# Kernel optimization log

Hardware: AMD Instinct MI355X
Metric: run time of the kernel (lower is better)

The kernel has to match this reference:

```python
import jax, jax.numpy as jnp
import numpy as np

B, T, C, H = 4, 2048, 1024, 16
HD = C // H

def setup_inputs() -> dict:
    key = jax.random.key(0)
    ks = jax.random.split(key, 9)
    s = 1.0 / np.sqrt(C)
    return {
        'x':  jax.random.normal(ks[0], (B, T, C), jnp.float32),
        'Wq': jax.random.normal(ks[1], (C, C), jnp.float32) * s,
        'bq': jnp.zeros((C,), jnp.float32),
        'Wk': jax.random.normal(ks[2], (C, C), jnp.float32) * s,
        'bk': jnp.zeros((C,), jnp.float32),
        'Wv': jax.random.normal(ks[3], (C, C), jnp.float32) * s,
        'bv': jnp.zeros((C,), jnp.float32),
        'Wo': jax.random.normal(ks[4], (C, C), jnp.float32) * s,
        'bo': jnp.zeros((C,), jnp.float32),
    }

def reference(x, Wq, bq, Wk, bk, Wv, bv, Wo, bo):
    Bx, Tx, Cx = x.shape
    # projections (torch Linear: x @ W.T + b); split heads -> (B,H,T,HD)
    def heads(y):
        return y.reshape(Bx, Tx, H, HD).transpose(0, 2, 1, 3)
    q = heads(x @ Wq.T + bq)
    k = heads(x @ Wk.T + bk)
    v = heads(x @ Wv.T + bv)
    # NOTE: original scales by 1/sqrt(embedding_dim), not head_dim
    scale = 1.0 / jnp.sqrt(jnp.asarray(Cx, x.dtype))
    att = jnp.einsum('bhqd,bhkd->bhqk', q, k) * scale
    mask = jnp.tril(jnp.ones((Tx, Tx), dtype=bool))
    att = jnp.where(mask, att, jnp.asarray(-jnp.inf, att.dtype))
    att = jax.nn.softmax(att, axis=-1)
    y = jnp.einsum('bhqk,bhkd->bhqd', att, v)
    y = y.transpose(0, 2, 1, 3).reshape(Bx, Tx, Cx)
    return y @ Wo.T + bo
```

## Files before the change

kernel.cpp:

```cpp
#include <hip/hip_runtime.h>
#include <hip/hip_bf16.h>
#include <stdint.h>

#define NB 4
#define NT 2048
#define NC 1024
#define NH 16
#define NHD 64
#define NM (NB*NT)

typedef __attribute__((ext_vector_type(8))) __bf16 bf16x8;
typedef __attribute__((ext_vector_type(4))) float floatx4;
typedef __attribute__((ext_vector_type(8))) unsigned short ushortx8;

#define AS1(p) ((const __attribute__((address_space(1))) void*)(p))
#define AS3(p) ((__attribute__((address_space(3))) void*)(p))

__device__ __forceinline__ unsigned short f2bf(float f) {
    union { float f; unsigned int u; } v; v.f = f;
    unsigned int u = v.u;
    return (unsigned short)((u + 0x7FFFu + ((u >> 16) & 1u)) >> 16);
}
__device__ __forceinline__ unsigned int pk2(float lo, float hi) {
    union { float f; unsigned int u; } a, b; a.f = hi; b.f = lo;
    return __builtin_amdgcn_perm(a.u, b.u, 0x07060302u);
}


__global__ void cast_all(const float* __restrict__ x,
                         const float* __restrict__ w0, const float* __restrict__ w1,
                         const float* __restrict__ w2, const float* __restrict__ w3,
                         unsigned short* __restrict__ xo,
                         unsigned short* __restrict__ o0, unsigned short* __restrict__ o1,
                         unsigned short* __restrict__ o2, unsigned short* __restrict__ o3)
{
    const int wid  = (blockIdx.x * blockDim.x + threadIdx.x) >> 6;
    const int lane = threadIdx.x & 63;
    const float* in; unsigned short* out; int tile;
    if (wid < 16384) { in = x; out = xo; tile = wid; }
    else {
        const int t = wid - 16384;
        tile = t & 2047;
        switch (t >> 11) {
            case 0: in = w0; out = o0; break;
            case 1: in = w1; out = o1; break;
            case 2: in = w2; out = o2; break;
            default: in = w3; out = o3; break;
        }
    }
    const int R = tile >> 5, C = tile & 31;
    const float* src = in + ((size_t)(R*16 + (lane >> 2)))*1024 + C*32 + (lane & 3)*8;
    const floatx4 v0 = *(const floatx4*)src;
    const floatx4 v1 = *(const floatx4*)(src + 4);
    ushortx8 o;
    o[0] = f2bf(v0[0]); o[1] = f2bf(v0[1]); o[2] = f2bf(v0[2]); o[3] = f2bf(v0[3]);
    o[4] = f2bf(v1[0]); o[5] = f2bf(v1[1]); o[6] = f2bf(v1[2]); o[7] = f2bf(v1[3]);
    *(ushortx8*)&out[(size_t)tile*512 + (((lane & 3)*16 + (lane >> 2)))*8] = o;
}

#define TM 128
#define TN 128
#define BK 32

template<int MODE>
__device__ __forceinline__ void gemm_core(
    const unsigned short* __restrict__ A,
    const unsigned short* __restrict__ W,
    const float* __restrict__ bias,
    void* __restrict__ Out,
    unsigned short* As, unsigned short* Bs,
    int m_base, int n_base, float oscale)
{
    const int tid  = threadIdx.x;
    const int lane = tid & 63;
    const int wv   = tid >> 6;
    const int quad = lane >> 4;
    const int l16  = lane & 15;
    const int wm = (wv >> 1) * 64;
    const int wn = (wv & 1) * 64;

    floatx4 acc[4][4];
    #pragma unroll
    for (int i = 0; i < 4; ++i)
        #pragma unroll
        for (int j = 0; j < 4; ++j)
            acc[i][j] = (floatx4){0.f, 0.f, 0.f, 0.f};

    const int kct = NC >> 5;

    const unsigned short* At = A + ((size_t)((m_base >> 4) + wv*2) * kct) * 512 + (size_t)lane*8;
    const unsigned short* Wt = W + ((size_t)((n_base >> 4) + wv*2) * kct) * 512 + (size_t)lane*8;
    const size_t rstride = (size_t)kct * 512;

    #pragma unroll
    for (int i = 0; i < 2; ++i) {
        __builtin_amdgcn_global_load_lds(AS1(At + i*rstride),
                                         AS3(&As[(wv*2 + i)*512]), 16, 0, 0);
        __builtin_amdgcn_global_load_lds(AS1(Wt + i*rstride),
                                         AS3(&Bs[(wv*2 + i)*512]), 16, 0, 0);
    }

    #pragma unroll 1
    for (int kt = 0; kt < 32; ++kt) {
        const int cur = (kt & 1) << 12;
        const int nxt = 4096 - cur;
        if (kt < 31) {
            #pragma unroll
            for (int i = 0; i < 2; ++i) {
                __builtin_amdgcn_global_load_lds(
                    AS1(At + (size_t)(kt+1)*512 + i*rstride),
                    AS3(&As[nxt + (wv*2 + i)*512]), 16, 0, 0);
                __builtin_amdgcn_global_load_lds(
                    AS1(Wt + (size_t)(kt+1)*512 + i*rstride),
                    AS3(&Bs[nxt + (wv*2 + i)*512]), 16, 0, 0);
            }
            asm volatile("s_waitcnt vmcnt(4)" ::: "memory");
        } else {
            asm volatile("s_waitcnt vmcnt(0)" ::: "memory");
        }
        __builtin_amdgcn_s_barrier();

        bf16x8 af[4], bfr[4];
        #pragma unroll
        for (int mi = 0; mi < 4; ++mi)
            af[mi] = *(const bf16x8*)&As[cur + ((wv >> 1)*4 + mi)*512 + lane*8];
        #pragma unroll
        for (int ni = 0; ni < 4; ++ni)
            bfr[ni] = *(const bf16x8*)&Bs[cur + ((wv & 1)*4 + ni)*512 + lane*8];

        #pragma unroll
        for (int mi = 0; mi < 4; ++mi)
            #pragma unroll
            for (int ni = 0; ni < 4; ++ni) {
                if (MODE == 1)
                    acc[mi][ni] = __builtin_amdgcn_mfma_f32_16x16x32_bf16(
                        bfr[ni], af[mi], acc[mi][ni], 0, 0, 0);
                else
                    acc[mi][ni] = __builtin_amdgcn_mfma_f32_16x16x32_bf16(
                        af[mi], bfr[ni], acc[mi][ni], 0, 0, 0);
            }
        __builtin_amdgcn_s_barrier();
    }

    #pragma unroll
    for (int mi = 0; mi < 4; ++mi) {
        #pragma unroll
        for (int ni = 0; ni < 4; ++ni) {
            if (MODE == 0) {
                const int col = n_base + wn + ni*16 + l16;
                const float bv = bias[col & 1023];
                #pragma unroll
                for (int r = 0; r < 4; ++r) {
                    const int row = m_base + wm + mi*16 + quad*4 + r;
                    ((float*)Out)[(size_t)row * NC + col] =
                        (acc[mi][ni][r] + bv) * oscale;
                }
            } else if (MODE == 1) {
                const int d0 = n_base + wn + ni*16 + quad*4;
                const int t  = m_base + wm + mi*16 + l16;
                const float4 b4 = *(const float4*)&bias[d0];
                const int bb = t >> 11, tt = t & (NT - 1);
                const int h  = (d0 >> 6) & (NH - 1), dd0 = d0 & 63;
                const int bh = bb * NH + h;
                const size_t idx0 =
                    ((size_t)((bh*128 + (tt >> 4))*2 + (dd0 >> 5)))*512
                    + (size_t)((((dd0 >> 3) & 3)*16 + (tt & 15))*8 + (dd0 & 7));
                ushort4 st;
                st.x = f2bf((acc[mi][ni][0] + b4.x) * oscale);
                st.y = f2bf((acc[mi][ni][1] + b4.y) * oscale);
                st.z = f2bf((acc[mi][ni][2] + b4.z) * oscale);
                st.w = f2bf((acc[mi][ni][3] + b4.w) * oscale);
                *(ushort4*)&((unsigned short*)Out)[idx0] = st;
            } else {
                const int col = n_base + wn + ni*16 + l16;
                const float bv = bias[col & 1023];
                const int row0 = m_base + wm + mi*16 + quad*4;
                const int bb = row0 >> 11, t0 = row0 & (NT - 1);
                const int h  = (col >> 6) & (NH - 1), hd = col & 63;
                const int bh = bb * NH + h;
                const int tk0 = t0 & 31;
                const int qv  = (tk0 >> 2) & 3;
                const int jv0 = (tk0 >> 4) << 2;
                const size_t idx0 =
                    ((size_t)((bh*64 + (t0 >> 5))*4 + (hd >> 4)))*512
                    + (size_t)((qv*16 + (hd & 15))*8 + jv0);
                ushort4 st;
                st.x = f2bf((acc[mi][ni][0] + bv) * oscale);
                st.y = f2bf((acc[mi][ni][1] + bv) * oscale);
                st.z = f2bf((acc[mi][ni][2] + bv) * oscale);
                st.w = f2bf((acc[mi][ni][3] + bv) * oscale);
                *(ushort4*)&((unsigned short*)Out)[idx0] = st;
            }
        }
    }
}

#define QSCALE (0.03125f * 1.44269504088896340736f)

__global__ __launch_bounds__(256) void gemm_qkv(
    const unsigned short* __restrict__ A,
    const unsigned short* __restrict__ Wq, const unsigned short* __restrict__ Wk,
    const unsigned short* __restrict__ Wv,
    const float* __restrict__ bq, const float* __restrict__ bk,
    const float* __restrict__ bv,
    unsigned short* __restrict__ Qo, unsigned short* __restrict__ Ko,
    unsigned short* __restrict__ Vo)
{
    __shared__ __align__(16) unsigned short As[2*TM*BK];
    __shared__ __align__(16) unsigned short Bs[2*TN*BK];
    const int m_base = blockIdx.x * TM;
    const int n_base = blockIdx.y * TN;
    gemm_core<1>(A, Wq, bq, Qo, As, Bs, m_base, n_base, QSCALE);
    gemm_core<1>(A, Wk, bk, Ko, As, Bs, m_base, n_base, 1.0f);
    gemm_core<2>(A, Wv, bv, Vo, As, Bs, m_base, n_base, 1.0f);
}

__global__ __launch_bounds__(256) void gemm_out(
    const unsigned short* __restrict__ A,
    const unsigned short* __restrict__ W,
    const float* __restrict__ bias,
    float* __restrict__ Out)
{
    __shared__ __align__(16) unsigned short As[2*TM*BK];
    __shared__ __align__(16) unsigned short Bs[2*TN*BK];
    gemm_core<0>(A, W, bias, Out, As, Bs, blockIdx.x * TM, blockIdx.y * TN, 1.0f);
}

__device__ __forceinline__ void attn_tile(
    const bf16x8 kf[4][2], const bf16x8 vf[4][2],
    const bf16x8 q[4], floatx4 o[2][4], float l[2],
    bool diag, bool skiphi, int q0, int j0, int quad, int l16)
{
    #pragma unroll
    for (int sub = 0; sub < 2; ++sub) {
        const bf16x8 qx0 = q[sub*2];
        const bf16x8 qx1 = q[sub*2 + 1];

        floatx4 s[4];
        __builtin_amdgcn_s_setprio(1);
        #pragma unroll
        for (int ct = 0; ct < 2; ++ct) {
            s[ct] = (floatx4){0.f,0.f,0.f,0.f};
            s[ct] = __builtin_amdgcn_mfma_f32_16x16x32_bf16(kf[ct][0], qx0, s[ct], 0,0,0);
            s[ct] = __builtin_amdgcn_mfma_f32_16x16x32_bf16(kf[ct][1], qx1, s[ct], 0,0,0);
        }
        if (!skiphi) {
            #pragma unroll
            for (int ct = 2; ct < 4; ++ct) {
                s[ct] = (floatx4){0.f,0.f,0.f,0.f};
                s[ct] = __builtin_amdgcn_mfma_f32_16x16x32_bf16(kf[ct][0], qx0, s[ct], 0,0,0);
                s[ct] = __builtin_amdgcn_mfma_f32_16x16x32_bf16(kf[ct][1], qx1, s[ct], 0,0,0);
            }
        }
        __builtin_amdgcn_s_setprio(0);

        float p[4][4];
        float psum[4];
        const int row = q0 + sub*16 + l16;
        #pragma unroll
        for (int ct = 0; ct < 2; ++ct) {
            if (!diag) {
                #pragma unroll
                for (int r = 0; r < 4; ++r)
                    p[ct][r] = __builtin_amdgcn_exp2f(s[ct][r]);
            } else {
                #pragma unroll
                for (int r = 0; r < 4; ++r) {
                    const int key = j0 + ct*16 + quad*4 + r;
                    p[ct][r] = (key <= row) ? __builtin_amdgcn_exp2f(s[ct][r]) : 0.f;
                }
            }
            psum[ct] = (p[ct][0] + p[ct][1]) + (p[ct][2] + p[ct][3]);
        }
        if (!skiphi) {
            #pragma unroll
            for (int ct = 2; ct < 4; ++ct) {
                if (!diag) {
                    #pragma unroll
                    for (int r = 0; r < 4; ++r)
                        p[ct][r] = __builtin_amdgcn_exp2f(s[ct][r]);
                } else {
                    #pragma unroll
                    for (int r = 0; r < 4; ++r) {
                        const int key = j0 + ct*16 + quad*4 + r;
                        p[ct][r] = (key <= row) ? __builtin_amdgcn_exp2f(s[ct][r]) : 0.f;
                    }
                }
                psum[ct] = (p[ct][0] + p[ct][1]) + (p[ct][2] + p[ct][3]);
            }
            l[sub] += (psum[0] + psum[1]) + (psum[2] + psum[3]);
        } else {
            l[sub] += psum[0] + psum[1];
        }

        union { bf16x8 v; unsigned int u[4]; } pf0;
        pf0.u[0] = pk2(p[0][0], p[0][1]); pf0.u[1] = pk2(p[0][2], p[0][3]);
        pf0.u[2] = pk2(p[1][0], p[1][1]); pf0.u[3] = pk2(p[1][2], p[1][3]);

        __builtin_amdgcn_s_setprio(1);
        #pragma unroll
        for (int nt = 0; nt < 4; ++nt)
            o[sub][nt] = __builtin_amdgcn_mfma_f32_16x16x32_bf16(vf[nt][0], pf0.v, o[sub][nt], 0,0,0);
        __builtin_amdgcn_s_setprio(0);

        if (!skiphi) {
            union { bf16x8 v; unsigned int u[4]; } pf1;
            pf1.u[0] = pk2(p[2][0], p[2][1]); pf1.u[1] = pk2(p[2][2], p[2][3]);
            pf1.u[2] = pk2(p[3][0], p[3][1]); pf1.u[3] = pk2(p[3][2], p[3][3]);
            __builtin_amdgcn_s_setprio(1);
            #pragma unroll
            for (int nt = 0; nt < 4; ++nt)
                o[sub][nt] = __builtin_amdgcn_mfma_f32_16x16x32_bf16(vf[nt][1], pf1.v, o[sub][nt], 0,0,0);
            __builtin_amdgcn_s_setprio(0);
        }
    }
}

__device__ __forceinline__ void attn_store(
    unsigned short* __restrict__ Y, const floatx4 o[2][4], const float l[2],
    int q0, int b, int h, int quad, int l16)
{
    float la = l[0], lb = l[1];
    la += __shfl_xor(la, 16); la += __shfl_xor(la, 32);
    lb += __shfl_xor(lb, 16); lb += __shfl_xor(lb, 32);
    const float ia = 1.0f / la, ib = 1.0f / lb;
    const size_t Rbase = (size_t)((b*NT + q0) >> 4);
    const int cg = (quad >> 1), co = (quad & 1)*4;
    #pragma unroll
    for (int nt = 0; nt < 4; ++nt) {
        const size_t base = ((Rbase*32 + h*2 + (nt >> 1))*512)
                          + (size_t)((((nt & 1)*2 + cg)*16 + l16)*8 + co);
        ushort4 wa, wb;
        wa.x = f2bf(o[0][nt][0]*ia); wa.y = f2bf(o[0][nt][1]*ia);
        wa.z = f2bf(o[0][nt][2]*ia); wa.w = f2bf(o[0][nt][3]*ia);
        wb.x = f2bf(o[1][nt][0]*ib); wb.y = f2bf(o[1][nt][1]*ib);
        wb.z = f2bf(o[1][nt][2]*ib); wb.w = f2bf(o[1][nt][3]*ib);
        *(ushort4*)&Y[base]         = wa;
        *(ushort4*)&Y[base + 16384] = wb;
    }
}

__device__ __forceinline__ void attn_pair(
    const unsigned short* __restrict__ Qf,
    const unsigned short* __restrict__ Kf,
    const unsigned short* __restrict__ Vf,
    unsigned short* __restrict__ Y,
    int bh, int stA, int stB, int lane)
{
    const int quad = lane >> 4, l16 = lane & 15;
    const int b = bh >> 4, h = bh & (NH - 1);
    const int q0A = stA * 32, q0B = stB * 32;
    const int FA = q0A >> 6, FB = q0B >> 6;
    const bool skA = (q0A & 32) == 0;
    const bool skB = (q0B & 32) == 0;

    const size_t qbA = ((size_t)(bh*128 + stA*2))*1024 + (size_t)lane*8;
    const size_t qbB = ((size_t)(bh*128 + stB*2))*1024 + (size_t)lane*8;
    bf16x8 qA[4], qB[4];
    qA[0] = *(const bf16x8*)&Qf[qbA];
    qA[1] = *(const bf16x8*)&Qf[qbA + 512];
    qA[2] = *(const bf16x8*)&Qf[qbA + 1024];
    qA[3] = *(const bf16x8*)&Qf[qbA + 1536];
    qB[0] = *(const bf16x8*)&Qf[qbB];
    qB[1] = *(const bf16x8*)&Qf[qbB + 512];
    qB[2] = *(const bf16x8*)&Qf[qbB + 1024];
    qB[3] = *(const bf16x8*)&Qf[qbB + 1536];

    const unsigned short* kp = Kf + (size_t)bh*131072 + (size_t)lane*8;
    const unsigned short* vp = Vf + (size_t)bh*131072 + (size_t)lane*8;

    floatx4 oA[2][4], oB[2][4];
    float lA[2] = {0.f, 0.f}, lB[2] = {0.f, 0.f};
    #pragma unroll
    for (int s2 = 0; s2 < 2; ++s2)
        #pragma unroll
        for (int nt = 0; nt < 4; ++nt) {
            oA[s2][nt] = (floatx4){0.f,0.f,0.f,0.f};
            oB[s2][nt] = (floatx4){0.f,0.f,0.f,0.f};
        }

    for (int f = 0; f <= FB; ++f) {
        const int j0 = f * 64;
        bf16x8 kf[4][2], vf[4][2];
        const unsigned short* kt = kp + (size_t)f * 4096;
        #pragma unroll
        for (int ct = 0; ct < 4; ++ct) {
            kf[ct][0] = *(const bf16x8*)&kt[ct*1024];
            kf[ct][1] = *(const bf16x8*)&kt[ct*1024 + 512];
        }
        const unsigned short* vt = vp + (size_t)f * 4096;
        #pragma unroll
        for (int nt = 0; nt < 4; ++nt) {
            vf[nt][0] = *(const bf16x8*)&vt[nt*512];
            vf[nt][1] = *(const bf16x8*)&vt[2048 + nt*512];
        }

        if (f <= FA)
            attn_tile(kf, vf, qA, oA, lA, f == FA, (f == FA) && skA,
                      q0A, j0, quad, l16);
        attn_tile(kf, vf, qB, oB, lB, f == FB, (f == FB) && skB,
                  q0B, j0, quad, l16);
    }

    attn_store(Y, oA, lA, q0A, b, h, quad, l16);
    attn_store(Y, oB, lB, q0B, b, h, quad, l16);
}

__global__ __launch_bounds__(256, 2) void flash_attn(
    const unsigned short* __restrict__ Qf,
    const unsigned short* __restrict__ Kf,
    const unsigned short* __restrict__ Vf,
    unsigned short* __restrict__ Y)
{
    const int tid  = threadIdx.x;
    const int wave = tid >> 6;
    const int lane = tid & 63;
    const int L  = blockIdx.x;
    const int bh = (L & 7) * 8 + ((L >> 3) & 7);
    const int x  = L >> 6;
    const int w  = x * 4 + wave;
    attn_pair(Qf, Kf, Vf, Y, bh, w, 63 - w, lane);
}

extern "C" void kernel_launch(void* const* d_in, const int* in_sizes, int n_in,
                              void* d_out, int out_size, void* d_ws, size_t ws_size,
                              hipStream_t stream) {
    const float* x  = (const float*)d_in[0];
    const float* Wq = (const float*)d_in[1];
    const float* bq = (const float*)d_in[2];
    const float* Wk = (const float*)d_in[3];
    const float* bk = (const float*)d_in[4];
    const float* Wv = (const float*)d_in[5];
    const float* bv = (const float*)d_in[6];
    const float* Wo = (const float*)d_in[7];
    const float* bo = (const float*)d_in[8];

    char* ws = (char*)d_ws;
    size_t off = 0;
    auto alloc = [&](size_t bytes) -> void* {
        void* p = ws + off;
        off += (bytes + 255) & ~(size_t)255;
        return p;
    };
    unsigned short* xb  = (unsigned short*)alloc((size_t)NM * NC * 2);
    unsigned short* Wqb = (unsigned short*)alloc((size_t)NC * NC * 2);
    unsigned short* Wkb = (unsigned short*)alloc((size_t)NC * NC * 2);
    unsigned short* Wvb = (unsigned short*)alloc((size_t)NC * NC * 2);
    unsigned short* Wob = (unsigned short*)alloc((size_t)NC * NC * 2);
    unsigned short* Qb  = (unsigned short*)alloc((size_t)NM * NC * 2);
    unsigned short* Kb  = (unsigned short*)alloc((size_t)NM * NC * 2);
    unsigned short* Vtb = (unsigned short*)alloc((size_t)NM * NC * 2);
    unsigned short* Yb  = (unsigned short*)alloc((size_t)NM * NC * 2);

    cast_all<<<(24576*64)/256, 256, 0, stream>>>(
        x, Wq, Wk, Wv, Wo, xb, Wqb, Wkb, Wvb, Wob);

    gemm_qkv<<<dim3(NM / TM, NC / TN), 256, 0, stream>>>(
        xb, Wqb, Wkb, Wvb, bq, bk, bv, Qb, Kb, Vtb);

    flash_attn<<<dim3(512), 256, 0, stream>>>(Qb, Kb, Vtb, Yb);

    gemm_out<<<dim3(NM / TM, NC / TN), 256, 0, stream>>>(Yb, Wob, bo, (float*)d_out);
}
```

Before: 233.4 us.

## Triple-buffer GEMM LDS pipeline and split QKV projections across grid blocks

The GEMM core moves from double to triple buffering in LDS. Loads are issued two k-steps ahead and the vmcnt waits are adjusted so more global-to-LDS latency overlaps with the MFMA work. The QKV kernel also launches three times as many blocks, each doing one of Q, K or V instead of all three in sequence, which raises parallelism and shortens each block's tail. The larger LDS footprint (48KB per block) may lower occupancy.

```diff
diff --git a/kernel.cpp b/kernel.cpp
--- a/kernel.cpp
+++ b/kernel.cpp
@@ -93,27 +93,34 @@
     const size_t rstride = (size_t)kct * 512;
 
     #pragma unroll
-    for (int i = 0; i < 2; ++i) {
-        __builtin_amdgcn_global_load_lds(AS1(At + i*rstride),
-                                         AS3(&As[(wv*2 + i)*512]), 16, 0, 0);
-        __builtin_amdgcn_global_load_lds(AS1(Wt + i*rstride),
-                                         AS3(&Bs[(wv*2 + i)*512]), 16, 0, 0);
-    }
-
+    for (int t = 0; t < 2; ++t) {
+        #pragma unroll
+        for (int i = 0; i < 2; ++i) {
+            __builtin_amdgcn_global_load_lds(
+                AS1(At + (size_t)t*512 + i*rstride),
+                AS3(&As[t*4096 + (wv*2 + i)*512]), 16, 0, 0);
+            __builtin_amdgcn_global_load_lds(
+                AS1(Wt + (size_t)t*512 + i*rstride),
+                AS3(&Bs[t*4096 + (wv*2 + i)*512]), 16, 0, 0);
+        }
+    }
+
+    int cb = 0;
     #pragma unroll 1
     for (int kt = 0; kt < 32; ++kt) {
-        const int cur = (kt & 1) << 12;
-        const int nxt = 4096 - cur;
-        if (kt < 31) {
+        if (kt < 30) {
+            int sb = cb + 8192; if (sb >= 12288) sb -= 12288;
             #pragma unroll
             for (int i = 0; i < 2; ++i) {
                 __builtin_amdgcn_global_load_lds(
-                    AS1(At + (size_t)(kt+1)*512 + i*rstride),
-                    AS3(&As[nxt + (wv*2 + i)*512]), 16, 0, 0);
+                    AS1(At + (size_t)(kt+2)*512 + i*rstride),
+                    AS3(&As[sb + (wv*2 + i)*512]), 16, 0, 0);
                 __builtin_amdgcn_global_load_lds(
-                    AS1(Wt + (size_t)(kt+1)*512 + i*rstride),
-                    AS3(&Bs[nxt + (wv*2 + i)*512]), 16, 0, 0);
-            }
+                    AS1(Wt + (size_t)(kt+2)*512 + i*rstride),
+                    AS3(&Bs[sb + (wv*2 + i)*512]), 16, 0, 0);
+            }
+            asm volatile("s_waitcnt vmcnt(8)" ::: "memory");
+        } else if (kt == 30) {
             asm volatile("s_waitcnt vmcnt(4)" ::: "memory");
         } else {
             asm volatile("s_waitcnt vmcnt(0)" ::: "memory");
@@ -123,10 +130,10 @@
         bf16x8 af[4], bfr[4];
         #pragma unroll
         for (int mi = 0; mi < 4; ++mi)
-            af[mi] = *(const bf16x8*)&As[cur + ((wv >> 1)*4 + mi)*512 + lane*8];
+            af[mi] = *(const bf16x8*)&As[cb + ((wv >> 1)*4 + mi)*512 + lane*8];
         #pragma unroll
         for (int ni = 0; ni < 4; ++ni)
-            bfr[ni] = *(const bf16x8*)&Bs[cur + ((wv & 1)*4 + ni)*512 + lane*8];
+            bfr[ni] = *(const bf16x8*)&Bs[cb + ((wv & 1)*4 + ni)*512 + lane*8];
 
         #pragma unroll
         for (int mi = 0; mi < 4; ++mi)
@@ -140,6 +147,7 @@
                         af[mi], bfr[ni], acc[mi][ni], 0, 0, 0);
             }
         __builtin_amdgcn_s_barrier();
+        cb += 4096; if (cb == 12288) cb = 0;
     }
 
     #pragma unroll
@@ -206,13 +214,17 @@
     unsigned short* __restrict__ Qo, unsigned short* __restrict__ Ko,
     unsigned short* __restrict__ Vo)
 {
-    __shared__ __align__(16) unsigned short As[2*TM*BK];
-    __shared__ __align__(16) unsigned short Bs[2*TN*BK];
+    __shared__ __align__(16) unsigned short As[3*TM*BK];
+    __shared__ __align__(16) unsigned short Bs[3*TN*BK];
+    const int wi = blockIdx.y >> 3;
+    const int n_base = (blockIdx.y & 7) * TN;
     const int m_base = blockIdx.x * TM;
-    const int n_base = blockIdx.y * TN;
-    gemm_core<1>(A, Wq, bq, Qo, As, Bs, m_base, n_base, QSCALE);
-    gemm_core<1>(A, Wk, bk, Ko, As, Bs, m_base, n_base, 1.0f);
-    gemm_core<2>(A, Wv, bv, Vo, As, Bs, m_base, n_base, 1.0f);
+    if (wi == 0)
+        gemm_core<1>(A, Wq, bq, Qo, As, Bs, m_base, n_base, QSCALE);
+    else if (wi == 1)
+        gemm_core<1>(A, Wk, bk, Ko, As, Bs, m_base, n_base, 1.0f);
+    else
+        gemm_core<2>(A, Wv, bv, Vo, As, Bs, m_base, n_base, 1.0f);
 }
 
 __global__ __launch_bounds__(256) void gemm_out(
@@ -221,8 +233,8 @@
     const float* __restrict__ bias,
     float* __restrict__ Out)
 {
-    __shared__ __align__(16) unsigned short As[2*TM*BK];
-    __shared__ __align__(16) unsigned short Bs[2*TN*BK];
+    __shared__ __align__(16) unsigned short As[3*TM*BK];
+    __shared__ __align__(16) unsigned short Bs[3*TN*BK];
     gemm_core<0>(A, W, bias, Out, As, Bs, blockIdx.x * TM, blockIdx.y * TN, 1.0f);
 }
 
@@ -455,7 +467,7 @@
     cast_all<<<(24576*64)/256, 256, 0, stream>>>(
         x, Wq, Wk, Wv, Wo, xb, Wqb, Wkb, Wvb, Wob);
 
-    gemm_qkv<<<dim3(NM / TM, NC / TN), 256, 0, stream>>>(
+    gemm_qkv<<<dim3(NM / TM, 24), 256, 0, stream>>>(
         xb, Wqb, Wkb, Wvb, bq, bk, bv, Qb, Kb, Vtb);
 
     flash_attn<<<dim3(512), 256, 0, stream>>>(Qb, Kb, Vtb, Yb);
```

Result: no change. 236.3 us (+1.2%).

## Share K/V tiles through double-buffered LDS in attention and split QKV GEMM grid

Applied to the files above, without the earlier changes.

The attention kernel previously had each wave load its own K/V tiles from global memory. Now the four waves of a block cooperatively stage each 64-key K/V tile into double-buffered LDS using global_load_lds, prefetching the next tile while the current one is computed, with barriers between steps. Separately, the QKV GEMM grid is tripled so each block computes only one of Q, K or V, giving more parallelism. The exchange is that waves in a block now synchronise and all run to the longest causal extent, adding barrier cost and idle iterations for waves with shorter ranges.

```diff
diff --git a/kernel.cpp b/kernel.cpp
--- a/kernel.cpp
+++ b/kernel.cpp
@@ -208,11 +208,15 @@
 {
     __shared__ __align__(16) unsigned short As[2*TM*BK];
     __shared__ __align__(16) unsigned short Bs[2*TN*BK];
+    const int wi = blockIdx.y >> 3;
+    const int n_base = (blockIdx.y & 7) * TN;
     const int m_base = blockIdx.x * TM;
-    const int n_base = blockIdx.y * TN;
-    gemm_core<1>(A, Wq, bq, Qo, As, Bs, m_base, n_base, QSCALE);
-    gemm_core<1>(A, Wk, bk, Ko, As, Bs, m_base, n_base, 1.0f);
-    gemm_core<2>(A, Wv, bv, Vo, As, Bs, m_base, n_base, 1.0f);
+    if (wi == 0)
+        gemm_core<1>(A, Wq, bq, Qo, As, Bs, m_base, n_base, QSCALE);
+    else if (wi == 1)
+        gemm_core<1>(A, Wk, bk, Ko, As, Bs, m_base, n_base, 1.0f);
+    else
+        gemm_core<2>(A, Wv, bv, Vo, As, Bs, m_base, n_base, 1.0f);
 }
 
 __global__ __launch_bounds__(256) void gemm_out(
@@ -340,17 +344,29 @@
     }
 }
 
-__device__ __forceinline__ void attn_pair(
+__global__ __launch_bounds__(256, 2) void flash_attn(
     const unsigned short* __restrict__ Qf,
     const unsigned short* __restrict__ Kf,
     const unsigned short* __restrict__ Vf,
-    unsigned short* __restrict__ Y,
-    int bh, int stA, int stB, int lane)
-{
+    unsigned short* __restrict__ Y)
+{
+    __shared__ __align__(16) unsigned short Ks[2][4096];
+    __shared__ __align__(16) unsigned short Vs[2][4096];
+
+    const int tid  = threadIdx.x;
+    const int wave = tid >> 6;
+    const int lane = tid & 63;
+    const int L  = blockIdx.x;
+    const int bh = (L & 7) * 8 + ((L >> 3) & 7);
+    const int x  = L >> 6;
+    const int w  = x * 4 + wave;
+    const int stA = w, stB = 63 - w;
+
     const int quad = lane >> 4, l16 = lane & 15;
     const int b = bh >> 4, h = bh & (NH - 1);
     const int q0A = stA * 32, q0B = stB * 32;
     const int FA = q0A >> 6, FB = q0B >> 6;
+    const int FBmax = (63 - 4*x) >> 1;
     const bool skA = (q0A & 32) == 0;
     const bool skB = (q0B & 32) == 0;
 
@@ -366,8 +382,8 @@
     qB[2] = *(const bf16x8*)&Qf[qbB + 1024];
     qB[3] = *(const bf16x8*)&Qf[qbB + 1536];
 
-    const unsigned short* kp = Kf + (size_t)bh*131072 + (size_t)lane*8;
-    const unsigned short* vp = Vf + (size_t)bh*131072 + (size_t)lane*8;
+    const unsigned short* kg = Kf + (size_t)bh*131072 + (size_t)wave*1024 + (size_t)lane*8;
+    const unsigned short* vg = Vf + (size_t)bh*131072 + (size_t)wave*1024 + (size_t)lane*8;
 
     floatx4 oA[2][4], oB[2][4];
     float lA[2] = {0.f, 0.f}, lB[2] = {0.f, 0.f};
@@ -379,47 +395,53 @@
             oB[s2][nt] = (floatx4){0.f,0.f,0.f,0.f};
         }
 
-    for (int f = 0; f <= FB; ++f) {
-        const int j0 = f * 64;
-        bf16x8 kf[4][2], vf[4][2];
-        const unsigned short* kt = kp + (size_t)f * 4096;
-        #pragma unroll
-        for (int ct = 0; ct < 4; ++ct) {
-            kf[ct][0] = *(const bf16x8*)&kt[ct*1024];
-            kf[ct][1] = *(const bf16x8*)&kt[ct*1024 + 512];
-        }
-        const unsigned short* vt = vp + (size_t)f * 4096;
-        #pragma unroll
-        for (int nt = 0; nt < 4; ++nt) {
-            vf[nt][0] = *(const bf16x8*)&vt[nt*512];
-            vf[nt][1] = *(const bf16x8*)&vt[2048 + nt*512];
-        }
-
-        if (f <= FA)
-            attn_tile(kf, vf, qA, oA, lA, f == FA, (f == FA) && skA,
-                      q0A, j0, quad, l16);
-        attn_tile(kf, vf, qB, oB, lB, f == FB, (f == FB) && skB,
-                  q0B, j0, quad, l16);
+    __builtin_amdgcn_global_load_lds(AS1(kg),       AS3(&Ks[0][wave*1024]),       16, 0, 0);
+    __builtin_amdgcn_global_load_lds(AS1(kg + 512), AS3(&Ks[0][wave*1024 + 512]), 16, 0, 0);
+    __builtin_amdgcn_global_load_lds(AS1(vg),       AS3(&Vs[0][wave*1024]),       16, 0, 0);
+    __builtin_amdgcn_global_load_lds(AS1(vg + 512), AS3(&Vs[0][wave*1024 + 512]), 16, 0, 0);
+
+    #pragma unroll 1
+    for (int f = 0; f <= FBmax; ++f) {
+        const int cur = f & 1;
+        if (f < FBmax) {
+            const int nb = cur ^ 1;
+            const unsigned short* kn = kg + (size_t)(f+1)*4096;
+            const unsigned short* vn = vg + (size_t)(f+1)*4096;
+            __builtin_amdgcn_global_load_lds(AS1(kn),       AS3(&Ks[nb][wave*1024]),       16, 0, 0);
+            __builtin_amdgcn_global_load_lds(AS1(kn + 512), AS3(&Ks[nb][wave*1024 + 512]), 16, 0, 0);
+            __builtin_amdgcn_global_load_lds(AS1(vn),       AS3(&Vs[nb][wave*1024]),       16, 0, 0);
+            __builtin_amdgcn_global_load_lds(AS1(vn + 512), AS3(&Vs[nb][wave*1024 + 512]), 16, 0, 0);
+            asm volatile("s_waitcnt vmcnt(4)" ::: "memory");
+        } else {
+            asm volatile("s_waitcnt vmcnt(0)" ::: "memory");
+        }
+        __builtin_amdgcn_s_barrier();
+
+        if (f <= FB) {
+            bf16x8 kf[4][2], vf[4][2];
+            #pragma unroll
+            for (int ct = 0; ct < 4; ++ct) {
+                kf[ct][0] = *(const bf16x8*)&Ks[cur][ct*1024 + lane*8];
+                kf[ct][1] = *(const bf16x8*)&Ks[cur][ct*1024 + 512 + lane*8];
+            }
+            #pragma unroll
+            for (int nt = 0; nt < 4; ++nt) {
+                vf[nt][0] = *(const bf16x8*)&Vs[cur][nt*512 + lane*8];
+                vf[nt][1] = *(const bf16x8*)&Vs[cur][2048 + nt*512 + lane*8];
+            }
+            const int j0 = f * 64;
+            if (f <= FA)
+                attn_tile(kf, vf, qA, oA, lA, f == FA, (f == FA) && skA,
+                          q0A, j0, quad, l16);
+            attn_tile(kf, vf, qB, oB, lB, f == FB, (f == FB) && skB,
+                      q0B, j0, quad, l16);
+        }
+        asm volatile("s_waitcnt lgkmcnt(0)" ::: "memory");
+        __builtin_amdgcn_s_barrier();
     }
 
     attn_store(Y, oA, lA, q0A, b, h, quad, l16);
     attn_store(Y, oB, lB, q0B, b, h, quad, l16);
-}
-
-__global__ __launch_bounds__(256, 2) void flash_attn(
-    const unsigned short* __restrict__ Qf,
-    const unsigned short* __restrict__ Kf,
-    const unsigned short* __restrict__ Vf,
-    unsigned short* __restrict__ Y)
-{
-    const int tid  = threadIdx.x;
-    const int wave = tid >> 6;
-    const int lane = tid & 63;
-    const int L  = blockIdx.x;
-    const int bh = (L & 7) * 8 + ((L >> 3) & 7);
-    const int x  = L >> 6;
-    const int w  = x * 4 + wave;
-    attn_pair(Qf, Kf, Vf, Y, bh, w, 63 - w, lane);
 }
 
 extern "C" void kernel_launch(void* const* d_in, const int* in_sizes, int n_in,
@@ -455,7 +477,7 @@
     cast_all<<<(24576*64)/256, 256, 0, stream>>>(
         x, Wq, Wk, Wv, Wo, xb, Wqb, Wkb, Wvb, Wob);
 
-    gemm_qkv<<<dim3(NM / TM, NC / TN), 256, 0, stream>>>(
+    gemm_qkv<<<dim3(NM / TM, 24), 256, 0, stream>>>(
         xb, Wqb, Wkb, Wvb, bq, bk, bv, Qb, Kb, Vtb);
 
     flash_attn<<<dim3(512), 256, 0, stream>>>(Qb, Kb, Vtb, Yb);
```

Result: slower. 243.1 us (+4.1%).
